# Performance work log

Hardware: AMD Instinct MI355X
Metric: run time of the kernel (lower is better)

## Reference

```python
import jax, jax.numpy as jnp
import numpy as np

B, D_IN, T, H = 256, 22, 1000, 64
G = 4 * H  # 256 gate rows, PyTorch order i,f,g,o


def _lstm_dir(x, w_ih, w_hh, b_ih, b_hh, reverse):
    # x: (B,T,D); w_ih: (4H,D); w_hh: (4H,H)
    xw = jnp.einsum('btd,gd->btg', x, w_ih) + b_ih + b_hh  # (B,T,4H)
    h0 = jnp.zeros((x.shape[0], H), x.dtype)

    def step(carry, xw_t):
        h, c = carry
        gates = xw_t + h @ w_hh.T
        i, f, g, o = jnp.split(gates, 4, axis=-1)
        i = jax.nn.sigmoid(i)
        f = jax.nn.sigmoid(f)
        g = jnp.tanh(g)
        o = jax.nn.sigmoid(o)
        c = f * c + i * g
        h = o * jnp.tanh(c)
        return (h, c), h

    _, hs = jax.lax.scan(step, (h0, h0), jnp.swapaxes(xw, 0, 1), reverse=reverse)
    return jnp.swapaxes(hs, 0, 1)  # (B,T,H), index t aligned with input t


def _bilstm_layer(x, w_ih, w_hh, b_ih, b_hh):
    hf = _lstm_dir(x, w_ih[0], w_hh[0], b_ih[0], b_hh[0], False)
    hb = _lstm_dir(x, w_ih[1], w_hh[1], b_ih[1], b_hh[1], True)
    return jnp.concatenate([hf, hb], axis=-1)  # (B,T,2H)


def setup_inputs() -> dict:
    key = jax.random.key(0)
    ks = jax.random.split(key, 8)
    s = 0.1  # keep gates out of deep saturation
    return {
        'x': jax.random.normal(ks[0], (B, D_IN, T), jnp.float32),
        'w_ih_first': jax.random.normal(ks[1], (2, G, D_IN), jnp.float32) * s,
        'w_ih_rest': jax.random.normal(ks[2], (3, 2, G, 2 * H), jnp.float32) * s,
        'w_hh': jax.random.normal(ks[3], (4, 2, G, H), jnp.float32) * s,
        'b_ih': jax.random.normal(ks[4], (4, 2, G), jnp.float32) * s,
        'b_hh': jax.random.normal(ks[5], (4, 2, G), jnp.float32) * s,
        'w_lin': jax.random.normal(ks[6], (54, 2 * H), jnp.float32) * s,
        'b_lin': jax.random.normal(ks[7], (54,), jnp.float32) * s,
    }


def reference(x, w_ih_first, w_ih_rest, w_hh, b_ih, b_hh, w_lin, b_lin):
    # x: (B, 22, T) -> (B, T, 22) as in torch .transpose(1, 2)
    out = jnp.swapaxes(x, 1, 2)
    # 4 stacked bidirectional layers: lstm1.l0, lstm1.l1, lstm2.l0, lstm2.l1
    out = _bilstm_layer(out, w_ih_first, w_hh[0], b_ih[0], b_hh[0])
    for i in range(3):
        out = _bilstm_layer(out, w_ih_rest[i], w_hh[i + 1], b_ih[i + 1], b_hh[i + 1])
    # last timestep -> linear head (B, 54)
    return out[:, -1, :] @ w_lin.T + b_lin
```

## Files before the change

kernel.cpp:

```cpp
#include <hip/hip_runtime.h>
#include <hip/hip_bf16.h>
#include <type_traits>

#define T_    1000
#define NB    256
#define HH    64
#define GG    256

typedef float f32x4 __attribute__((ext_vector_type(4)));
typedef __bf16 bf16x8 __attribute__((ext_vector_type(8)));

__device__ __forceinline__ void barrier_lds() {
    asm volatile("s_waitcnt lgkmcnt(0)\n\ts_barrier" ::: "memory");
}

__device__ __forceinline__ float fast_sigmoid(float x) {
    float e = __expf(-x);
    return __builtin_amdgcn_rcpf(1.f + e);
}
__device__ __forceinline__ float fast_tanh(float x) {
    x = fmaxf(x, -15.f);
    float e = __expf(-2.f * x);
    return (1.f - e) * __builtin_amdgcn_rcpf(1.f + e);
}
__device__ __forceinline__ float bf2f(unsigned short u) {
    return __builtin_bit_cast(float, (unsigned)u << 16);
}

__global__ void prep_w(const float* __restrict__ wihf, const float* __restrict__ wihr,
                       const float* __restrict__ whh, const float* __restrict__ bih,
                       const float* __restrict__ bhh,
                       __bf16* __restrict__ w0H, __bf16* __restrict__ w0L,
                       __bf16* __restrict__ wrH, __bf16* __restrict__ whH,
                       float* __restrict__ bias, float* __restrict__ w0f) {
    int i = blockIdx.x * 256 + threadIdx.x;
    if (i < 2 * GG * 32) {
        int k = i & 31, gd = i >> 5;
        float w = (k < 22) ? wihf[gd * 22 + k] : 0.f;
        __bf16 h = (__bf16)w;
        w0H[i] = h; w0L[i] = (__bf16)(w - (float)h);
        w0f[i] = w;
    }
    if (i < 3 * 2 * GG * 128) wrH[i] = (__bf16)wihr[i];
    if (i < 4 * 2 * GG * HH)  whH[i] = (__bf16)whh[i];
    if (i < 4 * 2 * GG)       bias[i] = bih[i] + bhh[i];
}

__global__ __launch_bounds__(256) void prep_x_ps(const float* __restrict__ x,
                                                 __bf16* __restrict__ xhi,
                                                 __bf16* __restrict__ xlo) {
    const int b = blockIdx.x;
    __shared__ float xs[22][104];
    for (int tc = 0; tc < 10; ++tc) {
        const int t0 = tc * 100;
        __syncthreads();
        for (int i = threadIdx.x; i < 22 * 100; i += 256) {
            int k = i / 100, t = i - k * 100;
            xs[k][t] = x[((size_t)b * 22 + k) * T_ + t0 + t];
        }
        __syncthreads();
        for (int i = threadIdx.x; i < 100 * 4; i += 256) {
            int t = i >> 2, p = i & 3;
            bf16x8 vh, vl;
            #pragma unroll
            for (int j = 0; j < 8; ++j) {
                int k = p * 8 + j;
                float f = (k < 22) ? xs[k][t] : 0.f;
                __bf16 h = (__bf16)f;
                vh[j] = h;
                vl[j] = (__bf16)(f - (float)h);
            }
            *(bf16x8*)(xhi + ((size_t)b * T_ + t0 + t) * 32 + p * 8) = vh;
            *(bf16x8*)(xlo + ((size_t)b * T_ + t0 + t) * 32 + p * 8) = vl;
        }
    }
}

__global__ __launch_bounds__(256) void prep_x_b(const float* __restrict__ x,
                                                __bf16* __restrict__ xp) {
    const int b = blockIdx.x;
    __shared__ float xs[22][104];
    for (int tc = 0; tc < 10; ++tc) {
        const int t0 = tc * 100;
        __syncthreads();
        for (int i = threadIdx.x; i < 22 * 100; i += 256) {
            int k = i / 100, t = i - k * 100;
            xs[k][t] = x[((size_t)b * 22 + k) * T_ + t0 + t];
        }
        __syncthreads();
        for (int i = threadIdx.x; i < 100 * 4; i += 256) {
            int t = i >> 2, p = i & 3;
            bf16x8 v;
            #pragma unroll
            for (int j = 0; j < 8; ++j) {
                int k = p * 8 + j;
                v[j] = (k < 22) ? (__bf16)xs[k][t] : (__bf16)0.f;
            }
            *(bf16x8*)(xp + ((size_t)b * T_ + t0 + t) * 32 + p * 8) = v;
        }
    }
}

template<int KCH, bool L0, bool FIN>
__global__ __launch_bounds__(256, 1) void fused_scan3(
    const __bf16* __restrict__ inA,
    const __bf16* __restrict__ inB,
    const __bf16* __restrict__ wihH,
    const __bf16* __restrict__ wihL,
    const __bf16* __restrict__ whhH,
    const float*  __restrict__ bias,
    __bf16* __restrict__ out,
    float* __restrict__ outF)
{
    const int dir = blockIdx.y;
    const int b0 = blockIdx.x * 2;
    const int tid = threadIdx.x;
    const int wv = tid >> 6, lane = tid & 63;
    const int j2 = lane & 15, q = lane >> 4;
    const int ch_l = j2 >> 3;
    const int u_l = j2 & 7;
    constexpr int KIN = KCH * 32;

    __shared__ __align__(16) __bf16 hbuf[2][2][80];

    const f32x4 Z4 = (f32x4){0.f, 0.f, 0.f, 0.f};

    bf16x8 wf[4][KCH], wfl[4][L0 ? KCH : 1];
    bf16x8 whf[4][2];
    float bgate[4];
    #pragma unroll
    for (int F = 0; F < 4; ++F) {
        const int g = (F * 4 + wv) * 16 + j2;
        bgate[F] = bias[dir * GG + g];
        #pragma unroll
        for (int ks = 0; ks < KCH; ++ks) {
            wf[F][ks] = *(const bf16x8*)(wihH + ((size_t)dir * GG + g) * KIN + ks * 32 + q * 8);
            if constexpr (L0)
                wfl[F][ks] = *(const bf16x8*)(wihL + ((size_t)dir * GG + g) * KIN + ks * 32 + q * 8);
        }
        #pragma unroll
        for (int ks = 0; ks < 2; ++ks)
            whf[F][ks] = *(const bf16x8*)(whhH + ((size_t)dir * GG + g) * HH + ks * 32 + q * 8);
    }
    if (tid < 64) {
        hbuf[1][0][tid] = (__bf16)0.f;
        hbuf[1][1][tid] = (__bf16)0.f;
    }
    __syncthreads();

    bf16x8 xfA[KCH], xfB[KCH];
    bf16x8 xlA[L0 ? KCH : 1], xlB[L0 ? KCH : 1];
    auto issue_x = [&](int grp, auto& dh, auto& dl) {
        int s = grp * 8 + u_l;
        if (s > T_ - 1) s = T_ - 1;
        int tt = dir ? (T_ - 1) - s : s;
        const __bf16* ph = inA + ((size_t)(b0 + ch_l) * T_ + tt) * KIN + q * 8;
        #pragma unroll
        for (int ks = 0; ks < KCH; ++ks)
            dh[ks] = *(const bf16x8*)(ph + ks * 32);
        if constexpr (L0) {
            const __bf16* pl = inB + ((size_t)(b0 + ch_l) * T_ + tt) * KIN + q * 8;
            #pragma unroll
            for (int ks = 0; ks < KCH; ++ks)
                dl[ks] = *(const bf16x8*)(pl + ks * 32);
        }
    };

    f32x4 Pu[4], Pn[4];
    #pragma unroll
    for (int F = 0; F < 4; ++F) { Pu[F] = Z4; Pn[F] = Z4; }
    issue_x(0, xfA, xlA);
    #pragma unroll
    for (int ks = 0; ks < KCH; ++ks)
        #pragma unroll
        for (int F = 0; F < 4; ++F)
            Pu[F] = __builtin_amdgcn_mfma_f32_16x16x32_bf16(xfA[ks], wf[F][ks], Pu[F], 0, 0, 0);
    if constexpr (L0) {
        #pragma unroll
        for (int ks = 0; ks < KCH; ++ks)
            #pragma unroll
            for (int F = 0; F < 4; ++F)
                Pu[F] = __builtin_amdgcn_mfma_f32_16x16x32_bf16(xlA[ks], wf[F][ks], Pu[F], 0, 0, 0);
        #pragma unroll
        for (int ks = 0; ks < KCH; ++ks)
            #pragma unroll
            for (int F = 0; F < 4; ++F)
                Pu[F] = __builtin_amdgcn_mfma_f32_16x16x32_bf16(xfA[ks], wfl[F][ks], Pu[F], 0, 0, 0);
    }
    #pragma unroll
    for (int F = 0; F < 4; ++F)
        #pragma unroll
        for (int r4 = 0; r4 < 4; ++r4)
            Pu[F][r4] += bgate[F];
    issue_x(1, xfB, xlB);

    float hsave[8];
    float creg = 0.f;

    auto FLUSH = [&](int g) {
        const int ch = q >> 1;
        const size_t col = (size_t)dir * HH + wv * 16 + j2;
        if (dir == 0) {
            __bf16* base = out + ((size_t)(b0 + ch) * T_ + g * 8) * 128 + col;
            #pragma unroll
            for (int u = 0; u < 8; ++u)
                if ((q & 1) == (u >> 2)) base[u * 128] = (__bf16)hsave[u];
            if constexpr (FIN)
                if (g == 124 && (q & 1) == 1)
                    outF[(size_t)(b0 + ch) * 128 + col] = hsave[7];
        } else {
            __bf16* base = out + ((size_t)(b0 + ch) * T_ + ((T_ - 1) - g * 8)) * 128 + col;
            #pragma unroll
            for (int u = 0; u < 8; ++u)
                if ((q & 1) == (u >> 2)) *(base - u * 128) = (__bf16)hsave[u];
            if constexpr (FIN)
                if (g == 0 && (q & 1) == 0)
                    outF[(size_t)(b0 + ch) * 128 + col] = hsave[0];
        }
    };

    auto GROUP = [&](int grp, auto& xcH, auto& xnH, auto& xcL, auto& xnL) {
        #pragma unroll
        for (int u = 0; u < 8; ++u) {
            const int rp = (u + 1) & 1;
            bf16x8 ah0 = *(const bf16x8*)&hbuf[rp][ch_l][q * 8];
            bf16x8 ah1 = *(const bf16x8*)&hbuf[rp][ch_l][32 + q * 8];

            if (u == 0 && grp > 0) FLUSH(grp - 1);

            if constexpr (!L0) {
                const int ks = u >> 1;
                const int Fb = (u & 1) * 2;
                Pn[Fb]     = __builtin_amdgcn_mfma_f32_16x16x32_bf16(xcH[ks], wf[Fb][ks],     Pn[Fb], 0, 0, 0);
                Pn[Fb + 1] = __builtin_amdgcn_mfma_f32_16x16x32_bf16(xcH[ks], wf[Fb + 1][ks], Pn[Fb + 1], 0, 0, 0);
            } else {
                if (u == 0) {
                    #pragma unroll
                    for (int F = 0; F < 4; ++F)
                        Pn[F] = __builtin_amdgcn_mfma_f32_16x16x32_bf16(xcH[0], wf[F][0], Pn[F], 0, 0, 0);
                } else if (u == 1) {
                    #pragma unroll
                    for (int F = 0; F < 4; ++F)
                        Pn[F] = __builtin_amdgcn_mfma_f32_16x16x32_bf16(xcL[0], wf[F][0], Pn[F], 0, 0, 0);
                } else if (u == 2) {
                    #pragma unroll
                    for (int F = 0; F < 4; ++F)
                        Pn[F] = __builtin_amdgcn_mfma_f32_16x16x32_bf16(xcH[0], wfl[F][0], Pn[F], 0, 0, 0);
                }
            }

            f32x4 R[4];
            #pragma unroll
            for (int F = 0; F < 4; ++F) {
                f32x4 t = __builtin_amdgcn_mfma_f32_16x16x32_bf16(ah0, whf[F][0], Z4, 0, 0, 0);
                R[F] = __builtin_amdgcn_mfma_f32_16x16x32_bf16(ah1, whf[F][1], t, 0, 0, 0);
            }

            if (u == 0) issue_x(grp + 2, xnH, xnL);

            const int r = u & 3;
            const int ch = q >> 1;
            float cold = creg;
            float iv = Pu[0][r] + R[0][r];
            float fv = Pu[1][r] + R[1][r];
            float gv = Pu[2][r] + R[2][r];
            float ov = Pu[3][r] + R[3][r];
            float cn = fast_sigmoid(fv) * cold + fast_sigmoid(iv) * fast_tanh(gv);
            float hn = fast_sigmoid(ov) * fast_tanh(cn);
            if (u == 3 || u == 7)
                creg = __builtin_bit_cast(float,
                        __builtin_amdgcn_ds_swizzle(__builtin_bit_cast(int, cn), 0x401F));
            else
                creg = cn;
            const bool owner = ((q & 1) == (u >> 2));
            if (owner) {
                hbuf[u & 1][ch][wv * 16 + j2] = (__bf16)hn;
                hsave[u] = hn;
            }
            barrier_lds();
        }
        #pragma unroll
        for (int F = 0; F < 4; ++F) {
            Pu[F] = Pn[F];
            Pn[F] = Z4;
            #pragma unroll
            for (int r4 = 0; r4 < 4; ++r4) Pu[F][r4] += bgate[F];
        }
    };

    for (int g2 = 0; g2 < 62; ++g2) {
        GROUP(g2 * 2,     xfB, xfA, xlB, xlA);
        GROUP(g2 * 2 + 1, xfA, xfB, xlA, xlB);
    }
    GROUP(124, xfB, xfA, xlB, xlA);
    FLUSH(124);
}

template<int KIN, typename TI, typename TO>
__global__ __launch_bounds__(256, 2) void scan_valu(
    const TI* __restrict__ in, const float* __restrict__ wih,
    const float* __restrict__ whh, const float* __restrict__ bias,
    TO* __restrict__ out)
{
    const int dir = blockIdx.y, bb = blockIdx.x, g = threadIdx.x;
    __shared__ __align__(16) float xs[8][KIN];
    __shared__ __align__(16) float act[256];
    __shared__ __align__(16) float hs[2][64];

    float wk[KIN], wr[64];
    {
        const float* wp = wih + (size_t)(dir * GG + g) * KIN;
        #pragma unroll
        for (int k4 = 0; k4 < KIN / 4; ++k4) {
            f32x4 v = *(const f32x4*)(wp + k4 * 4);
            wk[k4 * 4 + 0] = v.x; wk[k4 * 4 + 1] = v.y;
            wk[k4 * 4 + 2] = v.z; wk[k4 * 4 + 3] = v.w;
        }
        const float* rp = whh + (size_t)(dir * GG + g) * HH;
        #pragma unroll
        for (int j4 = 0; j4 < 16; ++j4) {
            f32x4 v = *(const f32x4*)(rp + j4 * 4);
            wr[j4 * 4 + 0] = v.x; wr[j4 * 4 + 1] = v.y;
            wr[j4 * 4 + 2] = v.z; wr[j4 * 4 + 3] = v.w;
        }
    }
    const float bg = bias[dir * GG + g];
    const bool is_g = (g >= 128 && g < 192);
    float c = 0.f;
    if (g < 64) hs[0][g] = 0.f;
    __syncthreads();

    float hreg[8];
    for (int ch = 0; ch < 125; ++ch) {
        if constexpr (KIN == 128) {
            int l = g * 4, u = l >> 7, k = l & 127;
            int s = ch * 8 + u, tt = dir ? (T_ - 1) - s : s;
            const TI* src = in + ((size_t)bb * T_ + tt) * 128 + k;
            f32x4 fv;
            if constexpr (std::is_same_v<TI, float>) fv = *(const f32x4*)src;
            else {
                ushort4 rv = *(const ushort4*)src;
                fv = (f32x4){bf2f(rv.x), bf2f(rv.y), bf2f(rv.z), bf2f(rv.w)};
            }
            *(f32x4*)&xs[u][k] = fv;
        } else {
            int u = g >> 5, k = g & 31;
            int s = ch * 8 + u, tt = dir ? (T_ - 1) - s : s;
            if constexpr (std::is_same_v<TI, float>)
                xs[u][k] = in[((size_t)bb * T_ + tt) * 32 + k];
            else
                xs[u][k] = bf2f(((const unsigned short*)in)[((size_t)bb * T_ + tt) * 32 + k]);
        }
        __syncthreads();
        #pragma unroll
        for (int u = 0; u < 8; ++u) {
            const int p = (ch * 8 + u) & 1;
            float a0 = bg, a1 = 0.f, a2 = 0.f, a3 = 0.f;
            #pragma unroll
            for (int k = 0; k < KIN; k += 4) {
                f32x4 xv = *(const f32x4*)&xs[u][k];
                a0 = fmaf(xv.x, wk[k + 0], a0); a1 = fmaf(xv.y, wk[k + 1], a1);
                a2 = fmaf(xv.z, wk[k + 2], a2); a3 = fmaf(xv.w, wk[k + 3], a3);
            }
            #pragma unroll
            for (int j = 0; j < 64; j += 4) {
                f32x4 hv = *(const f32x4*)&hs[p][j];
                a0 = fmaf(hv.x, wr[j + 0], a0); a1 = fmaf(hv.y, wr[j + 1], a1);
                a2 = fmaf(hv.z, wr[j + 2], a2); a3 = fmaf(hv.w, wr[j + 3], a3);
            }
            float a = (a0 + a1) + (a2 + a3);
            act[g] = is_g ? fast_tanh(a) : fast_sigmoid(a);
            __syncthreads();
            if (g < 64) {
                float iv = act[g], fv = act[64 + g], gv = act[128 + g], ov = act[192 + g];
                c = fmaf(fv, c, iv * gv);
                float hn = ov * fast_tanh(c);
                hs[p ^ 1][g] = hn;
                hreg[u] = hn;
            }
            __syncthreads();
        }
        if (g < 64) {
            #pragma unroll
            for (int u = 0; u < 8; ++u) {
                int s = ch * 8 + u, tt = dir ? (T_ - 1) - s : s;
                out[((size_t)bb * T_ + tt) * 128 + dir * HH + g] = (TO)hreg[u];
            }
        }
    }
}

__global__ __launch_bounds__(64) void head_last(
    const float* __restrict__ hl, const float* __restrict__ wlin,
    const float* __restrict__ blin, float* __restrict__ outp) {
    const int b = blockIdx.x, tid = threadIdx.x;
    __shared__ float hv[128];
    hv[tid] = hl[(size_t)b * 128 + tid];
    hv[64 + tid] = hl[(size_t)b * 128 + 64 + tid];
    __syncthreads();
    if (tid < 54) {
        float a = blin[tid];
        #pragma unroll 4
        for (int j = 0; j < 128; ++j) a = fmaf(hv[j], wlin[tid * 128 + j], a);
        outp[b * 54 + tid] = a;
    }
}

template<typename TI>
__global__ __launch_bounds__(64) void head_kernel(
    const TI* __restrict__ fin, const float* __restrict__ wlin,
    const float* __restrict__ blin, float* __restrict__ outp) {
    const int b = blockIdx.x, tid = threadIdx.x;
    __shared__ float hv[128];
    #pragma unroll
    for (int rr = 0; rr < 2; ++rr) {
        int j = rr * 64 + tid;
        hv[j] = (float)fin[((size_t)b * T_ + (T_ - 1)) * 128 + j];
    }
    __syncthreads();
    if (tid < 54) {
        float a = blin[tid];
        #pragma unroll 4
        for (int j = 0; j < 128; ++j) a = fmaf(hv[j], wlin[tid * 128 + j], a);
        outp[b * 54 + tid] = a;
    }
}

extern "C" void kernel_launch(void* const* d_in, const int* in_sizes, int n_in,
                              void* d_out, int out_size, void* d_ws, size_t ws_size,
                              hipStream_t stream) {
    const float* x    = (const float*)d_in[0];
    const float* wihf = (const float*)d_in[1];
    const float* wihr = (const float*)d_in[2];
    const float* whh  = (const float*)d_in[3];
    const float* bih  = (const float*)d_in[4];
    const float* bhh  = (const float*)d_in[5];
    const float* wlin = (const float*)d_in[6];
    const float* blin = (const float*)d_in[7];
    float* outp = (float*)d_out;

    char* ws = (char*)d_ws;
    const size_t PB = (size_t)NB * T_ * 128 * sizeof(__bf16);
    const size_t PX = (size_t)NB * T_ * 32 * sizeof(__bf16);
    const size_t HL = (size_t)NB * 128 * sizeof(float);
    const size_t WSZ = 794624;
    const bool primary = ws_size >= 2 * PB + 2 * PX + HL + WSZ;

    char* sw = primary ? (ws + 2 * PB + 2 * PX + HL) : (ws + 2 * PB);
    __bf16* w0H  = (__bf16*)(sw);
    __bf16* w0L  = (__bf16*)(sw + 32768);
    __bf16* wrH  = (__bf16*)(sw + 65536);
    __bf16* whH  = (__bf16*)(sw + 458752);
    float*  bias = (float*) (sw + 720896);
    float*  w0f  = (float*) (sw + 729088);

    prep_w<<<768, 256, 0, stream>>>(wihf, wihr, whh, bih, bhh,
                                    w0H, w0L, wrH, whH, bias, w0f);

    if (primary) {
        __bf16* A   = (__bf16*)ws;
        __bf16* B   = (__bf16*)(ws + PB);
        __bf16* xhi = (__bf16*)(ws + 2 * PB);
        __bf16* xlo = (__bf16*)(ws + 2 * PB + PX);
        float*  hl  = (float*)(ws + 2 * PB + 2 * PX);
        prep_x_ps<<<NB, 256, 0, stream>>>(x, xhi, xlo);
        const dim3 sgrid(NB / 2, 2);
        fused_scan3<1, true,  false><<<sgrid, 256, 0, stream>>>(xhi, xlo, w0H, w0L, whH, bias, A, nullptr);
        fused_scan3<4, false, false><<<sgrid, 256, 0, stream>>>(A, nullptr, wrH, nullptr,
            whH + 32768, bias + 512, B, nullptr);
        fused_scan3<4, false, false><<<sgrid, 256, 0, stream>>>(B, nullptr, wrH + 65536, nullptr,
            whH + 65536, bias + 1024, A, nullptr);
        fused_scan3<4, false, true><<<sgrid, 256, 0, stream>>>(A, nullptr, wrH + 131072, nullptr,
            whH + 98304, bias + 1536, B, hl);
        head_last<<<NB, 64, 0, stream>>>(hl, wlin, blin, outp);
    } else {
        __bf16* A = (__bf16*)ws;
        __bf16* B = (__bf16*)(ws + PB);
        __bf16* xp = (__bf16*)ws;
        prep_x_b<<<NB, 256, 0, stream>>>(x, xp);
        const dim3 vgrid(NB, 2);
        scan_valu<32, __bf16, __bf16><<<vgrid, 256, 0, stream>>>(xp, w0f, whh, bias, B);
        scan_valu<128, __bf16, __bf16><<<vgrid, 256, 0, stream>>>(B, wihr,          whh + 32768, bias + 512,  A);
        scan_valu<128, __bf16, __bf16><<<vgrid, 256, 0, stream>>>(A, wihr + 65536,  whh + 65536, bias + 1024, B);
        scan_valu<128, __bf16, __bf16><<<vgrid, 256, 0, stream>>>(B, wihr + 131072, whh + 98304, bias + 1536, A);
        head_kernel<__bf16><<<NB, 64, 0, stream>>>(A, wlin, blin, outp);
    }
}
```

Before: 1.182 ms.

## Stage input weights in LDS and fold bias/input projection into MFMA accumulators

For the non-first layers, the input-to-hidden weight fragments move from registers into LDS and are prefetched one step ahead. This is meant to cut VGPR pressure. The precomputed input-projection accumulator plus bias now seeds the recurrent MFMA chain, which removes the separate adds. Double-buffered accumulators and h-save arrays replace the copy-and-reset at the end of each group. The output flush is spread across the eight steps instead of run as a burst, and the x prefetch is moved to steps 1–2. In exchange the kernel adds LDS reads on the serial critical path and uses about 70KB of LDS, which may lower occupancy.

```diff
diff --git a/kernel.cpp b/kernel.cpp
--- a/kernel.cpp
+++ b/kernel.cpp
@@ -122,21 +122,34 @@
     constexpr int KIN = KCH * 32;
 
     __shared__ __align__(16) __bf16 hbuf[2][2][80];
+    __shared__ __align__(16) __bf16 wlds[L0 ? 16 : 256 * 136];
 
     const f32x4 Z4 = (f32x4){0.f, 0.f, 0.f, 0.f};
 
-    bf16x8 wf[4][KCH], wfl[4][L0 ? KCH : 1];
+    if constexpr (!L0) {
+        const __bf16* src = wihH + (size_t)dir * GG * KIN;
+        #pragma unroll
+        for (int it = 0; it < 16; ++it) {
+            int idx = it * 256 + tid;
+            int row = idx >> 4, cw = idx & 15;
+            *(bf16x8*)(&wlds[row * 136 + cw * 8]) = *(const bf16x8*)(src + (size_t)idx * 8);
+        }
+    }
+
+    bf16x8 wf[L0 ? 4 : 1][L0 ? KCH : 1], wfl[4][L0 ? KCH : 1];
     bf16x8 whf[4][2];
-    float bgate[4];
+    f32x4 bias4[4];
     #pragma unroll
     for (int F = 0; F < 4; ++F) {
         const int g = (F * 4 + wv) * 16 + j2;
-        bgate[F] = bias[dir * GG + g];
-        #pragma unroll
-        for (int ks = 0; ks < KCH; ++ks) {
-            wf[F][ks] = *(const bf16x8*)(wihH + ((size_t)dir * GG + g) * KIN + ks * 32 + q * 8);
-            if constexpr (L0)
+        float bg = bias[dir * GG + g];
+        bias4[F] = (f32x4){bg, bg, bg, bg};
+        if constexpr (L0) {
+            #pragma unroll
+            for (int ks = 0; ks < KCH; ++ks) {
+                wf[F][ks] = *(const bf16x8*)(wihH + ((size_t)dir * GG + g) * KIN + ks * 32 + q * 8);
                 wfl[F][ks] = *(const bf16x8*)(wihL + ((size_t)dir * GG + g) * KIN + ks * 32 + q * 8);
+            }
         }
         #pragma unroll
         for (int ks = 0; ks < 2; ++ks)
@@ -147,6 +160,8 @@
         hbuf[1][1][tid] = (__bf16)0.f;
     }
     __syncthreads();
+
+    const int wbase = (wv * 16 + j2) * 136 + q * 8;
 
     bf16x8 xfA[KCH], xfB[KCH];
     bf16x8 xlA[L0 ? KCH : 1], xlB[L0 ? KCH : 1];
@@ -166,105 +181,112 @@
         }
     };
 
-    f32x4 Pu[4], Pn[4];
+    f32x4 PuA[4], PuB[4];
     #pragma unroll
-    for (int F = 0; F < 4; ++F) { Pu[F] = Z4; Pn[F] = Z4; }
+    for (int F = 0; F < 4; ++F) { PuA[F] = bias4[F]; PuB[F] = bias4[F]; }
     issue_x(0, xfA, xlA);
-    #pragma unroll
-    for (int ks = 0; ks < KCH; ++ks)
+    if constexpr (L0) {
         #pragma unroll
         for (int F = 0; F < 4; ++F)
-            Pu[F] = __builtin_amdgcn_mfma_f32_16x16x32_bf16(xfA[ks], wf[F][ks], Pu[F], 0, 0, 0);
-    if constexpr (L0) {
+            PuA[F] = __builtin_amdgcn_mfma_f32_16x16x32_bf16(xfA[0], wf[F][0], PuA[F], 0, 0, 0);
+        #pragma unroll
+        for (int F = 0; F < 4; ++F)
+            PuA[F] = __builtin_amdgcn_mfma_f32_16x16x32_bf16(xlA[0], wf[F][0], PuA[F], 0, 0, 0);
+        #pragma unroll
+        for (int F = 0; F < 4; ++F)
+            PuA[F] = __builtin_amdgcn_mfma_f32_16x16x32_bf16(xfA[0], wfl[F][0], PuA[F], 0, 0, 0);
+    } else {
         #pragma unroll
         for (int ks = 0; ks < KCH; ++ks)
             #pragma unroll
-            for (int F = 0; F < 4; ++F)
-                Pu[F] = __builtin_amdgcn_mfma_f32_16x16x32_bf16(xlA[ks], wf[F][ks], Pu[F], 0, 0, 0);
-        #pragma unroll
-        for (int ks = 0; ks < KCH; ++ks)
-            #pragma unroll
-            for (int F = 0; F < 4; ++F)
-                Pu[F] = __builtin_amdgcn_mfma_f32_16x16x32_bf16(xfA[ks], wfl[F][ks], Pu[F], 0, 0, 0);
-    }
-    #pragma unroll
-    for (int F = 0; F < 4; ++F)
-        #pragma unroll
-        for (int r4 = 0; r4 < 4; ++r4)
-            Pu[F][r4] += bgate[F];
+            for (int F = 0; F < 4; ++F) {
+                bf16x8 w = *(const bf16x8*)&wlds[wbase + F * 8704 + ks * 32];
+                PuA[F] = __builtin_amdgcn_mfma_f32_16x16x32_bf16(xfA[ks], w, PuA[F], 0, 0, 0);
+            }
+    }
     issue_x(1, xfB, xlB);
 
-    float hsave[8];
+    bf16x8 w00, w01, wp[2][2];
+    if constexpr (!L0) {
+        w00 = *(const bf16x8*)&wlds[wbase];
+        w01 = *(const bf16x8*)&wlds[wbase + 8704];
+    }
+
+    float hsA[8], hsB[8];
     float creg = 0.f;
 
-    auto FLUSH = [&](int g) {
+    auto GROUP = [&](int grp, auto& xcH, auto& xnH, auto& xcL, auto& xnL,
+                     f32x4 (&Pc)[4], f32x4 (&Pnx)[4],
+                     float (&hsC)[8], float (&hsP)[8]) {
+        const bool doflush = grp > 0;
         const int ch = q >> 1;
-        const size_t col = (size_t)dir * HH + wv * 16 + j2;
-        if (dir == 0) {
-            __bf16* base = out + ((size_t)(b0 + ch) * T_ + g * 8) * 128 + col;
-            #pragma unroll
-            for (int u = 0; u < 8; ++u)
-                if ((q & 1) == (u >> 2)) base[u * 128] = (__bf16)hsave[u];
-            if constexpr (FIN)
-                if (g == 124 && (q & 1) == 1)
-                    outF[(size_t)(b0 + ch) * 128 + col] = hsave[7];
-        } else {
-            __bf16* base = out + ((size_t)(b0 + ch) * T_ + ((T_ - 1) - g * 8)) * 128 + col;
-            #pragma unroll
-            for (int u = 0; u < 8; ++u)
-                if ((q & 1) == (u >> 2)) *(base - u * 128) = (__bf16)hsave[u];
-            if constexpr (FIN)
-                if (g == 0 && (q & 1) == 0)
-                    outF[(size_t)(b0 + ch) * 128 + col] = hsave[0];
-        }
-    };
-
-    auto GROUP = [&](int grp, auto& xcH, auto& xnH, auto& xcL, auto& xnL) {
+        const ptrdiff_t fstep = dir ? -128 : 128;
+        const int bt = dir ? (T_ - 1) - (grp - 1) * 8 : (grp - 1) * 8;
+        __bf16* fb = out + ((size_t)(b0 + ch) * T_ + bt) * 128
+                         + (size_t)dir * HH + wv * 16 + j2;
         #pragma unroll
         for (int u = 0; u < 8; ++u) {
             const int rp = (u + 1) & 1;
             bf16x8 ah0 = *(const bf16x8*)&hbuf[rp][ch_l][q * 8];
             bf16x8 ah1 = *(const bf16x8*)&hbuf[rp][ch_l][32 + q * 8];
 
-            if (u == 0 && grp > 0) FLUSH(grp - 1);
+            if constexpr (!L0) {
+                if (u < 7) {
+                    const int un = u + 1, ksn = un >> 1, Fbn = (un & 1) * 2;
+                    wp[un & 1][0] = *(const bf16x8*)&wlds[wbase + Fbn * 8704 + ksn * 32];
+                    wp[un & 1][1] = *(const bf16x8*)&wlds[wbase + (Fbn + 1) * 8704 + ksn * 32];
+                }
+            }
+
+            if (doflush && ((q & 1) == (u >> 2))) {
+                fb[(ptrdiff_t)u * fstep] = (__bf16)hsP[u];
+                if constexpr (FIN)
+                    if (u == 0 && dir == 1 && grp == 1)
+                        outF[(size_t)(b0 + ch) * 128 + HH + wv * 16 + j2] = hsP[0];
+            }
+
+            if constexpr (L0) {
+                if (u == 1) issue_x(grp + 2, xnH, xnL);
+            } else {
+                if (u == 1 || u == 2) issue_x(grp + 2, xnH, xnL);
+            }
 
             if constexpr (!L0) {
                 const int ks = u >> 1;
                 const int Fb = (u & 1) * 2;
-                Pn[Fb]     = __builtin_amdgcn_mfma_f32_16x16x32_bf16(xcH[ks], wf[Fb][ks],     Pn[Fb], 0, 0, 0);
-                Pn[Fb + 1] = __builtin_amdgcn_mfma_f32_16x16x32_bf16(xcH[ks], wf[Fb + 1][ks], Pn[Fb + 1], 0, 0, 0);
+                bf16x8 pw0 = (u == 0) ? w00 : wp[u & 1][0];
+                bf16x8 pw1 = (u == 0) ? w01 : wp[u & 1][1];
+                Pnx[Fb]     = __builtin_amdgcn_mfma_f32_16x16x32_bf16(xcH[ks], pw0, Pnx[Fb], 0, 0, 0);
+                Pnx[Fb + 1] = __builtin_amdgcn_mfma_f32_16x16x32_bf16(xcH[ks], pw1, Pnx[Fb + 1], 0, 0, 0);
             } else {
                 if (u == 0) {
                     #pragma unroll
                     for (int F = 0; F < 4; ++F)
-                        Pn[F] = __builtin_amdgcn_mfma_f32_16x16x32_bf16(xcH[0], wf[F][0], Pn[F], 0, 0, 0);
+                        Pnx[F] = __builtin_amdgcn_mfma_f32_16x16x32_bf16(xcH[0], wf[F][0], Pnx[F], 0, 0, 0);
                 } else if (u == 1) {
                     #pragma unroll
                     for (int F = 0; F < 4; ++F)
-                        Pn[F] = __builtin_amdgcn_mfma_f32_16x16x32_bf16(xcL[0], wf[F][0], Pn[F], 0, 0, 0);
+                        Pnx[F] = __builtin_amdgcn_mfma_f32_16x16x32_bf16(xcL[0], wf[F][0], Pnx[F], 0, 0, 0);
                 } else if (u == 2) {
                     #pragma unroll
                     for (int F = 0; F < 4; ++F)
-                        Pn[F] = __builtin_amdgcn_mfma_f32_16x16x32_bf16(xcH[0], wfl[F][0], Pn[F], 0, 0, 0);
+                        Pnx[F] = __builtin_amdgcn_mfma_f32_16x16x32_bf16(xcH[0], wfl[F][0], Pnx[F], 0, 0, 0);
                 }
             }
 
             f32x4 R[4];
             #pragma unroll
             for (int F = 0; F < 4; ++F) {
-                f32x4 t = __builtin_amdgcn_mfma_f32_16x16x32_bf16(ah0, whf[F][0], Z4, 0, 0, 0);
+                f32x4 t = __builtin_amdgcn_mfma_f32_16x16x32_bf16(ah0, whf[F][0], Pc[F], 0, 0, 0);
                 R[F] = __builtin_amdgcn_mfma_f32_16x16x32_bf16(ah1, whf[F][1], t, 0, 0, 0);
             }
 
-            if (u == 0) issue_x(grp + 2, xnH, xnL);
-
             const int r = u & 3;
-            const int ch = q >> 1;
             float cold = creg;
-            float iv = Pu[0][r] + R[0][r];
-            float fv = Pu[1][r] + R[1][r];
-            float gv = Pu[2][r] + R[2][r];
-            float ov = Pu[3][r] + R[3][r];
+            float iv = R[0][r];
+            float fv = R[1][r];
+            float gv = R[2][r];
+            float ov = R[3][r];
             float cn = fast_sigmoid(fv) * cold + fast_sigmoid(iv) * fast_tanh(gv);
             float hn = fast_sigmoid(ov) * fast_tanh(cn);
             if (u == 3 || u == 7)
@@ -275,25 +297,33 @@
             const bool owner = ((q & 1) == (u >> 2));
             if (owner) {
                 hbuf[u & 1][ch][wv * 16 + j2] = (__bf16)hn;
-                hsave[u] = hn;
+                hsC[u] = hn;
             }
             barrier_lds();
         }
         #pragma unroll
-        for (int F = 0; F < 4; ++F) {
-            Pu[F] = Pn[F];
-            Pn[F] = Z4;
-            #pragma unroll
-            for (int r4 = 0; r4 < 4; ++r4) Pu[F][r4] += bgate[F];
-        }
+        for (int F = 0; F < 4; ++F) Pc[F] = bias4[F];
     };
 
     for (int g2 = 0; g2 < 62; ++g2) {
-        GROUP(g2 * 2,     xfB, xfA, xlB, xlA);
-        GROUP(g2 * 2 + 1, xfA, xfB, xlA, xlB);
-    }
-    GROUP(124, xfB, xfA, xlB, xlA);
-    FLUSH(124);
+        GROUP(g2 * 2,     xfB, xfA, xlB, xlA, PuA, PuB, hsA, hsB);
+        GROUP(g2 * 2 + 1, xfA, xfB, xlA, xlB, PuB, PuA, hsB, hsA);
+    }
+    GROUP(124, xfB, xfA, xlB, xlA, PuA, PuB, hsA, hsB);
+
+    {
+        const int ch = q >> 1;
+        const ptrdiff_t fstep = dir ? -128 : 128;
+        const int bt = dir ? (T_ - 1) - 124 * 8 : 124 * 8;
+        __bf16* fb = out + ((size_t)(b0 + ch) * T_ + bt) * 128
+                         + (size_t)dir * HH + wv * 16 + j2;
+        #pragma unroll
+        for (int u = 0; u < 8; ++u)
+            if ((q & 1) == (u >> 2)) fb[(ptrdiff_t)u * fstep] = (__bf16)hsA[u];
+        if constexpr (FIN)
+            if (dir == 0 && ((q & 1) == 1))
+                outF[(size_t)(b0 + ch) * 128 + wv * 16 + j2] = hsA[7];
+    }
 }
 
 template<int KIN, typename TI, typename TO>
```

New measurement: 1.259 ms. +6.5%, slower.

## Process one batch element per block with 16-step groups, two blocks per CU

Applied to the files above, without the earlier changes.

Each scan block now handles a single batch element instead of two, so the grid doubles to 512 blocks, and launch bounds allow two blocks per CU. The per-step timestep tiling widens from 8 to 16 steps per group, with a new lane-to-timestep mapping and a cross-half bpermute to carry the cell state. The intent is more blocks in flight on the serial recurrence to hide the latency of each step. In exchange each MFMA now does half-useful work, since only 16 rows are meaningful per group, and register pressure is capped by the occupancy-2 bound.

```diff
diff --git a/kernel.cpp b/kernel.cpp
--- a/kernel.cpp
+++ b/kernel.cpp
@@ -102,7 +102,7 @@
 }
 
 template<int KCH, bool L0, bool FIN>
-__global__ __launch_bounds__(256, 1) void fused_scan3(
+__global__ __launch_bounds__(256, 2) void fused_scan1c(
     const __bf16* __restrict__ inA,
     const __bf16* __restrict__ inB,
     const __bf16* __restrict__ wihH,
@@ -113,15 +113,15 @@
     float* __restrict__ outF)
 {
     const int dir = blockIdx.y;
-    const int b0 = blockIdx.x * 2;
+    const int bb = blockIdx.x;
     const int tid = threadIdx.x;
     const int wv = tid >> 6, lane = tid & 63;
     const int j2 = lane & 15, q = lane >> 4;
-    const int ch_l = j2 >> 3;
-    const int u_l = j2 & 7;
+    const int u_l = j2 ^ ((j2 & 8) >> 1);
+    const int bpidx = (lane ^ 32) << 2;
     constexpr int KIN = KCH * 32;
 
-    __shared__ __align__(16) __bf16 hbuf[2][2][80];
+    __shared__ __align__(16) __bf16 hbuf[2][80];
 
     const f32x4 Z4 = (f32x4){0.f, 0.f, 0.f, 0.f};
 
@@ -142,24 +142,21 @@
         for (int ks = 0; ks < 2; ++ks)
             whf[F][ks] = *(const bf16x8*)(whhH + ((size_t)dir * GG + g) * HH + ks * 32 + q * 8);
     }
-    if (tid < 64) {
-        hbuf[1][0][tid] = (__bf16)0.f;
-        hbuf[1][1][tid] = (__bf16)0.f;
-    }
+    if (tid < 64) hbuf[1][tid] = (__bf16)0.f;
     __syncthreads();
 
     bf16x8 xfA[KCH], xfB[KCH];
     bf16x8 xlA[L0 ? KCH : 1], xlB[L0 ? KCH : 1];
     auto issue_x = [&](int grp, auto& dh, auto& dl) {
-        int s = grp * 8 + u_l;
+        int s = grp * 16 + u_l;
         if (s > T_ - 1) s = T_ - 1;
         int tt = dir ? (T_ - 1) - s : s;
-        const __bf16* ph = inA + ((size_t)(b0 + ch_l) * T_ + tt) * KIN + q * 8;
+        const __bf16* ph = inA + ((size_t)bb * T_ + tt) * KIN + q * 8;
         #pragma unroll
         for (int ks = 0; ks < KCH; ++ks)
             dh[ks] = *(const bf16x8*)(ph + ks * 32);
         if constexpr (L0) {
-            const __bf16* pl = inB + ((size_t)(b0 + ch_l) * T_ + tt) * KIN + q * 8;
+            const __bf16* pl = inB + ((size_t)bb * T_ + tt) * KIN + q * 8;
             #pragma unroll
             for (int ks = 0; ks < KCH; ++ks)
                 dl[ks] = *(const bf16x8*)(pl + ks * 32);
@@ -194,59 +191,53 @@
             Pu[F][r4] += bgate[F];
     issue_x(1, xfB, xlB);
 
-    float hsave[8];
+    float hsave[4];
     float creg = 0.f;
 
-    auto FLUSH = [&](int g) {
-        const int ch = q >> 1;
+    const int sbase = (q == 0) ? 0 : (q == 1) ? 4 : (q == 2) ? 12 : 8;
+
+    auto FLUSH = [&](int g, bool tail) {
+        if (tail && q >= 2) return;
+        const int s0 = g * 16 + sbase;
         const size_t col = (size_t)dir * HH + wv * 16 + j2;
         if (dir == 0) {
-            __bf16* base = out + ((size_t)(b0 + ch) * T_ + g * 8) * 128 + col;
-            #pragma unroll
-            for (int u = 0; u < 8; ++u)
-                if ((q & 1) == (u >> 2)) base[u * 128] = (__bf16)hsave[u];
-            if constexpr (FIN)
-                if (g == 124 && (q & 1) == 1)
-                    outF[(size_t)(b0 + ch) * 128 + col] = hsave[7];
+            __bf16* base = out + ((size_t)bb * T_ + s0) * 128 + col;
+            #pragma unroll
+            for (int r = 0; r < 4; ++r) base[r * 128] = (__bf16)hsave[r];
         } else {
-            __bf16* base = out + ((size_t)(b0 + ch) * T_ + ((T_ - 1) - g * 8)) * 128 + col;
-            #pragma unroll
-            for (int u = 0; u < 8; ++u)
-                if ((q & 1) == (u >> 2)) *(base - u * 128) = (__bf16)hsave[u];
-            if constexpr (FIN)
-                if (g == 0 && (q & 1) == 0)
-                    outF[(size_t)(b0 + ch) * 128 + col] = hsave[0];
+            __bf16* base = out + ((size_t)bb * T_ + ((T_ - 1) - s0)) * 128 + col;
+            #pragma unroll
+            for (int r = 0; r < 4; ++r) *(base - r * 128) = (__bf16)hsave[r];
+        }
+        if constexpr (FIN) {
+            if (!tail) {
+                if (g == 0 && dir == 1 && q == 0)
+                    outF[(size_t)bb * 128 + col] = hsave[0];
+            } else {
+                if (dir == 0 && q == 1)
+                    outF[(size_t)bb * 128 + col] = hsave[3];
+            }
         }
     };
 
     auto GROUP = [&](int grp, auto& xcH, auto& xnH, auto& xcL, auto& xnL) {
         #pragma unroll
-        for (int u = 0; u < 8; ++u) {
-            const int rp = (u + 1) & 1;
-            bf16x8 ah0 = *(const bf16x8*)&hbuf[rp][ch_l][q * 8];
-            bf16x8 ah1 = *(const bf16x8*)&hbuf[rp][ch_l][32 + q * 8];
-
-            if (u == 0 && grp > 0) FLUSH(grp - 1);
+        for (int u = 0; u < 16; ++u) {
+            bf16x8 ah0 = *(const bf16x8*)&hbuf[(u + 1) & 1][q * 8];
+            bf16x8 ah1 = *(const bf16x8*)&hbuf[(u + 1) & 1][32 + q * 8];
+
+            if (u == 0 && grp > 0) FLUSH(grp - 1, false);
 
             if constexpr (!L0) {
-                const int ks = u >> 1;
-                const int Fb = (u & 1) * 2;
-                Pn[Fb]     = __builtin_amdgcn_mfma_f32_16x16x32_bf16(xcH[ks], wf[Fb][ks],     Pn[Fb], 0, 0, 0);
-                Pn[Fb + 1] = __builtin_amdgcn_mfma_f32_16x16x32_bf16(xcH[ks], wf[Fb + 1][ks], Pn[Fb + 1], 0, 0, 0);
+                Pn[u & 3] = __builtin_amdgcn_mfma_f32_16x16x32_bf16(
+                    xcH[u >> 2], wf[u & 3][u >> 2], Pn[u & 3], 0, 0, 0);
             } else {
-                if (u == 0) {
-                    #pragma unroll
-                    for (int F = 0; F < 4; ++F)
-                        Pn[F] = __builtin_amdgcn_mfma_f32_16x16x32_bf16(xcH[0], wf[F][0], Pn[F], 0, 0, 0);
-                } else if (u == 1) {
-                    #pragma unroll
-                    for (int F = 0; F < 4; ++F)
-                        Pn[F] = __builtin_amdgcn_mfma_f32_16x16x32_bf16(xcL[0], wf[F][0], Pn[F], 0, 0, 0);
-                } else if (u == 2) {
-                    #pragma unroll
-                    for (int F = 0; F < 4; ++F)
-                        Pn[F] = __builtin_amdgcn_mfma_f32_16x16x32_bf16(xcH[0], wfl[F][0], Pn[F], 0, 0, 0);
-                }
+                if (u < 4)
+                    Pn[u] = __builtin_amdgcn_mfma_f32_16x16x32_bf16(xcH[0], wf[u][0], Pn[u], 0, 0, 0);
+                else if (u < 8)
+                    Pn[u - 4] = __builtin_amdgcn_mfma_f32_16x16x32_bf16(xcL[0], wf[u - 4][0], Pn[u - 4], 0, 0, 0);
+                else if (u < 12)
+                    Pn[u - 8] = __builtin_amdgcn_mfma_f32_16x16x32_bf16(xcH[0], wfl[u - 8][0], Pn[u - 8], 0, 0, 0);
             }
 
             f32x4 R[4];
@@ -259,7 +250,7 @@
             if (u == 0) issue_x(grp + 2, xnH, xnL);
 
             const int r = u & 3;
-            const int ch = q >> 1;
+            const int qo = (u ^ ((u & 8) >> 1)) >> 2;
             float cold = creg;
             float iv = Pu[0][r] + R[0][r];
             float fv = Pu[1][r] + R[1][r];
@@ -267,15 +258,17 @@
             float ov = Pu[3][r] + R[3][r];
             float cn = fast_sigmoid(fv) * cold + fast_sigmoid(iv) * fast_tanh(gv);
             float hn = fast_sigmoid(ov) * fast_tanh(cn);
-            if (u == 3 || u == 7)
+            if (u == 3 || u == 11)
                 creg = __builtin_bit_cast(float,
                         __builtin_amdgcn_ds_swizzle(__builtin_bit_cast(int, cn), 0x401F));
+            else if (u == 7 || u == 15)
+                creg = __builtin_bit_cast(float,
+                        __builtin_amdgcn_ds_bpermute(bpidx, __builtin_bit_cast(int, cn)));
             else
                 creg = cn;
-            const bool owner = ((q & 1) == (u >> 2));
-            if (owner) {
-                hbuf[u & 1][ch][wv * 16 + j2] = (__bf16)hn;
-                hsave[u] = hn;
+            if (q == qo) {
+                hbuf[u & 1][wv * 16 + j2] = (__bf16)hn;
+                hsave[r] = hn;
             }
             barrier_lds();
         }
@@ -288,12 +281,12 @@
         }
     };
 
-    for (int g2 = 0; g2 < 62; ++g2) {
+    for (int g2 = 0; g2 < 31; ++g2) {
         GROUP(g2 * 2,     xfB, xfA, xlB, xlA);
         GROUP(g2 * 2 + 1, xfA, xfB, xlA, xlB);
     }
-    GROUP(124, xfB, xfA, xlB, xlA);
-    FLUSH(124);
+    GROUP(62, xfB, xfA, xlB, xlA);
+    FLUSH(62, true);
 }
 
 template<int KIN, typename TI, typename TO>
@@ -464,13 +457,13 @@
         __bf16* xlo = (__bf16*)(ws + 2 * PB + PX);
         float*  hl  = (float*)(ws + 2 * PB + 2 * PX);
         prep_x_ps<<<NB, 256, 0, stream>>>(x, xhi, xlo);
-        const dim3 sgrid(NB / 2, 2);
-        fused_scan3<1, true,  false><<<sgrid, 256, 0, stream>>>(xhi, xlo, w0H, w0L, whH, bias, A, nullptr);
-        fused_scan3<4, false, false><<<sgrid, 256, 0, stream>>>(A, nullptr, wrH, nullptr,
+        const dim3 sgrid(NB, 2);
+        fused_scan1c<1, true,  false><<<sgrid, 256, 0, stream>>>(xhi, xlo, w0H, w0L, whH, bias, A, nullptr);
+        fused_scan1c<4, false, false><<<sgrid, 256, 0, stream>>>(A, nullptr, wrH, nullptr,
             whH + 32768, bias + 512, B, nullptr);
-        fused_scan3<4, false, false><<<sgrid, 256, 0, stream>>>(B, nullptr, wrH + 65536, nullptr,
+        fused_scan1c<4, false, false><<<sgrid, 256, 0, stream>>>(B, nullptr, wrH + 65536, nullptr,
             whH + 65536, bias + 1024, A, nullptr);
-        fused_scan3<4, false, true><<<sgrid, 256, 0, stream>>>(A, nullptr, wrH + 131072, nullptr,
+        fused_scan1c<4, false, true><<<sgrid, 256, 0, stream>>>(A, nullptr, wrH + 131072, nullptr,
             whH + 98304, bias + 1536, B, hl);
         head_last<<<NB, 64, 0, stream>>>(hl, wlin, blin, outp);
     } else {
```

Result: slower. 1.409 ms (+19.2%).

## Spread h stores and x prefetch across steps and fold input gates into MFMA accumulator

Applied to the files above, without the earlier changes.

The group's flush of saved hidden states now runs one store per timestep inside the 8-step loop instead of a burst at the first step, using double-buffered save arrays. Next-group x loads are split into halves issued at different steps. The precomputed input-projection gates are passed as the MFMA accumulator initial value, which removes the separate adds. The aim is to smooth memory traffic and shorten the serial per-step critical path, in exchange for more live registers.

```diff
diff --git a/kernel.cpp b/kernel.cpp
--- a/kernel.cpp
+++ b/kernel.cpp
@@ -165,6 +165,15 @@
                 dl[ks] = *(const bf16x8*)(pl + ks * 32);
         }
     };
+    auto issue_x_half = [&](int grp, auto& dh, int half) {
+        int s = grp * 8 + u_l;
+        if (s > T_ - 1) s = T_ - 1;
+        int tt = dir ? (T_ - 1) - s : s;
+        const __bf16* ph = inA + ((size_t)(b0 + ch_l) * T_ + tt) * KIN + q * 8;
+        #pragma unroll
+        for (int ks = 0; ks < 2; ++ks)
+            dh[half * 2 + ks] = *(const bf16x8*)(ph + (half * 2 + ks) * 32);
+    };
 
     f32x4 Pu[4], Pn[4];
     #pragma unroll
@@ -194,39 +203,59 @@
             Pu[F][r4] += bgate[F];
     issue_x(1, xfB, xlB);
 
-    float hsave[8];
+    float hsA[8], hsB[8];
     float creg = 0.f;
 
-    auto FLUSH = [&](int g) {
+    auto FLUSH = [&](int g, float (&hs)[8]) {
         const int ch = q >> 1;
         const size_t col = (size_t)dir * HH + wv * 16 + j2;
         if (dir == 0) {
             __bf16* base = out + ((size_t)(b0 + ch) * T_ + g * 8) * 128 + col;
             #pragma unroll
             for (int u = 0; u < 8; ++u)
-                if ((q & 1) == (u >> 2)) base[u * 128] = (__bf16)hsave[u];
+                if ((q & 1) == (u >> 2)) base[u * 128] = (__bf16)hs[u];
             if constexpr (FIN)
                 if (g == 124 && (q & 1) == 1)
-                    outF[(size_t)(b0 + ch) * 128 + col] = hsave[7];
+                    outF[(size_t)(b0 + ch) * 128 + col] = hs[7];
         } else {
             __bf16* base = out + ((size_t)(b0 + ch) * T_ + ((T_ - 1) - g * 8)) * 128 + col;
             #pragma unroll
             for (int u = 0; u < 8; ++u)
-                if ((q & 1) == (u >> 2)) *(base - u * 128) = (__bf16)hsave[u];
+                if ((q & 1) == (u >> 2)) *(base - u * 128) = (__bf16)hs[u];
             if constexpr (FIN)
                 if (g == 0 && (q & 1) == 0)
-                    outF[(size_t)(b0 + ch) * 128 + col] = hsave[0];
+                    outF[(size_t)(b0 + ch) * 128 + col] = hs[0];
         }
     };
 
-    auto GROUP = [&](int grp, auto& xcH, auto& xnH, auto& xcL, auto& xnL) {
+    auto GROUP = [&](int grp, auto& xcH, auto& xnH, auto& xcL, auto& xnL,
+                     float (&hsC)[8], float (&hsP)[8]) {
+        const bool doflush = grp > 0;
+        const int gprev = doflush ? grp - 1 : 0;
+        const int ch = q >> 1;
+        const ptrdiff_t fstep = dir ? -128 : 128;
+        const int bt = dir ? (T_ - 1) - gprev * 8 : gprev * 8;
+        __bf16* fb = out + ((size_t)(b0 + ch) * T_ + bt) * 128
+                         + (size_t)dir * HH + wv * 16 + j2;
         #pragma unroll
         for (int u = 0; u < 8; ++u) {
             const int rp = (u + 1) & 1;
             bf16x8 ah0 = *(const bf16x8*)&hbuf[rp][ch_l][q * 8];
             bf16x8 ah1 = *(const bf16x8*)&hbuf[rp][ch_l][32 + q * 8];
 
-            if (u == 0 && grp > 0) FLUSH(grp - 1);
+            if (doflush && ((q & 1) == (u >> 2))) {
+                fb[(ptrdiff_t)u * fstep] = (__bf16)hsP[u];
+                if constexpr (FIN)
+                    if (dir == 1 && grp == 1 && u == 0)
+                        outF[(size_t)(b0 + ch) * 128 + HH + wv * 16 + j2] = hsP[0];
+            }
+
+            if constexpr (L0) {
+                if (u == 1) issue_x(grp + 2, xnH, xnL);
+            } else {
+                if (u == 1) issue_x_half(grp + 2, xnH, 0);
+                if (u == 2) issue_x_half(grp + 2, xnH, 1);
+            }
 
             if constexpr (!L0) {
                 const int ks = u >> 1;
@@ -252,19 +281,16 @@
             f32x4 R[4];
             #pragma unroll
             for (int F = 0; F < 4; ++F) {
-                f32x4 t = __builtin_amdgcn_mfma_f32_16x16x32_bf16(ah0, whf[F][0], Z4, 0, 0, 0);
+                f32x4 t = __builtin_amdgcn_mfma_f32_16x16x32_bf16(ah0, whf[F][0], Pu[F], 0, 0, 0);
                 R[F] = __builtin_amdgcn_mfma_f32_16x16x32_bf16(ah1, whf[F][1], t, 0, 0, 0);
             }
 
-            if (u == 0) issue_x(grp + 2, xnH, xnL);
-
             const int r = u & 3;
-            const int ch = q >> 1;
             float cold = creg;
-            float iv = Pu[0][r] + R[0][r];
-            float fv = Pu[1][r] + R[1][r];
-            float gv = Pu[2][r] + R[2][r];
-            float ov = Pu[3][r] + R[3][r];
+            float iv = R[0][r];
+            float fv = R[1][r];
+            float gv = R[2][r];
+            float ov = R[3][r];
             float cn = fast_sigmoid(fv) * cold + fast_sigmoid(iv) * fast_tanh(gv);
             float hn = fast_sigmoid(ov) * fast_tanh(cn);
             if (u == 3 || u == 7)
@@ -275,7 +301,7 @@
             const bool owner = ((q & 1) == (u >> 2));
             if (owner) {
                 hbuf[u & 1][ch][wv * 16 + j2] = (__bf16)hn;
-                hsave[u] = hn;
+                hsC[u] = hn;
             }
             barrier_lds();
         }
@@ -289,11 +315,11 @@
     };
 
     for (int g2 = 0; g2 < 62; ++g2) {
-        GROUP(g2 * 2,     xfB, xfA, xlB, xlA);
-        GROUP(g2 * 2 + 1, xfA, xfB, xlA, xlB);
-    }
-    GROUP(124, xfB, xfA, xlB, xlA);
-    FLUSH(124);
+        GROUP(g2 * 2,     xfB, xfA, xlB, xlA, hsA, hsB);
+        GROUP(g2 * 2 + 1, xfA, xfB, xlA, xlB, hsB, hsA);
+    }
+    GROUP(124, xfB, xfA, xlB, xlA, hsA, hsB);
+    FLUSH(124, hsA);
 }
 
 template<int KIN, typename TI, typename TO>
```

Measured after the change: 1.296 ms. 9.6% more time.
